# Optimization experiments

Hardware: AMD Instinct MI355X
Metric: run time of the kernel (lower is better)

Reference implementation:

```python
import jax, jax.numpy as jnp
import numpy as np

N, F, E, B, D = 100000, 256, 128, 10000, 32
GAMMA, ZETA = -0.1, 1.1  # hard-concrete stretch params of L0Dense


def setup_inputs() -> dict:
    key = jax.random.key(0)
    ks = jax.random.split(key, 12)
    return {
        "nodes": jax.random.randint(ks[0], (B,), 0, N),
        "neigh_idx": jax.random.randint(ks[1], (B, D), 0, N),
        "neigh_mask": jax.random.bernoulli(ks[2], 0.9, (B, D)),
        "feature": jax.random.normal(ks[3], (N, F), jnp.float32),
        "W": jax.random.normal(ks[4], (F, E), jnp.float32) * 0.05,
        "b": jnp.zeros((E,), jnp.float32),
        "qz_loga": jax.random.normal(ks[5], (F,), jnp.float32),
        "att1_w": jax.random.normal(ks[6], (2 * E, E), jnp.float32) * 0.05,
        "att1_b": jnp.zeros((E,), jnp.float32),
        "att2_w": jax.random.normal(ks[7], (E, E), jnp.float32) * 0.05,
        "att2_b": jnp.zeros((E,), jnp.float32),
        "att3_w": jax.random.normal(ks[8], (E, 1), jnp.float32) * 0.05,
        "att3_b": jnp.zeros((1,), jnp.float32),
    }


def reference(nodes, neigh_idx, neigh_mask, feature, W, b, qz_loga,
              att1_w, att1_b, att2_w, att2_b, att3_w, att3_b):
    # L0Dense, deterministic (eval) hard-concrete gate on input dims
    z = jnp.clip(jax.nn.sigmoid(qz_loga) * (ZETA - GAMMA) + GAMMA, 0.0, 1.0)
    We = W * z[:, None]                                  # [F, E]

    node_feat = feature[nodes] @ We + b                   # [B, E]
    neigh_feat = feature[neigh_idx] @ We + b              # [B, D, E]

    # GraphRec-style attention MLP over (neighbor, center) pairs
    h = jnp.concatenate(
        [neigh_feat, jnp.broadcast_to(node_feat[:, None, :], neigh_feat.shape)],
        axis=-1)                                          # [B, D, 2E]
    h = jax.nn.relu(h @ att1_w + att1_b)
    h = jax.nn.relu(h @ att2_w + att2_b)
    scores = (h @ att3_w + att3_b)[..., 0]                # [B, D]
    scores = jnp.where(neigh_mask, scores, -1e30)
    att = jax.nn.softmax(scores, axis=-1)                 # [B, D]

    agg = jnp.einsum('bd,bde->be', att, neigh_feat)       # weighted sum
    has_neigh = neigh_mask.any(axis=-1, keepdims=True)
    return jnp.where(has_neigh, agg, node_feat)           # n==0 fallback
```

## Files before the change

kernel.cpp:

```cpp
#include <hip/hip_runtime.h>
#include <hip/hip_bf16.h>
#include <math.h>

#define NN 100000
#define FF 256
#define EE 128
#define BB_ 10000
#define DD 32

typedef __attribute__((ext_vector_type(8))) short short8;
typedef __attribute__((ext_vector_type(4))) float f32x4;

__device__ __forceinline__ short f2bf(float f) {
  __hip_bfloat16 h = __float2bfloat16(f);
  union { __hip_bfloat16 h; short s; } u; u.h = h;
  return u.s;
}
__device__ __forceinline__ float bf2f(short s) {
  union { unsigned u; float f; } v;
  v.u = ((unsigned)(unsigned short)s) << 16;
  return v.f;
}

__global__ __launch_bounds__(256) void k_prep(
    const float* __restrict__ W, const float* __restrict__ qz,
    const float* __restrict__ a1w, const float* __restrict__ a2w,
    short* __restrict__ WeT, short* __restrict__ a1wTn,
    short* __restrict__ a1wTc, short* __restrict__ w2T) {
  int i = blockIdx.x * 256 + threadIdx.x;
  if (i < 32768) {
    int e = i >> 8, f = i & 255;
    float g = qz[f];
    float s = 1.0f / (1.0f + expf(-g));
    float z = fminf(fmaxf(s * 1.2f - 0.1f, 0.0f), 1.0f);
    WeT[e * 256 + f] = f2bf(W[f * 128 + e] * z);
  } else if (i < 49152) {
    int t = i - 32768; int n = t >> 7, k = t & 127;
    a1wTn[n * 128 + k] = f2bf(a1w[k * 128 + n]);
  } else if (i < 65536) {
    int t = i - 49152; int n = t >> 7, k = t & 127;
    a1wTc[n * 128 + k] = f2bf(a1w[(128 + k) * 128 + n]);
  } else if (i < 81920) {
    int t = i - 65536; int n = t >> 7, k = t & 127;
    w2T[n * 128 + k] = f2bf(a2w[k * 128 + n]);
  }
}

template <int K, bool AF32, bool OUTBF16>
__global__ __launch_bounds__(256) void k_mm(
    const void* __restrict__ Ap, const short* __restrict__ BT,
    const float* __restrict__ bias, const int* __restrict__ idx,
    void* __restrict__ Cp, int M) {
  __shared__ short As[128 * 64];
  __shared__ short Bs[128 * 64];
  const int tid = threadIdx.x;
  const int mb = blockIdx.x * 128;
  const int wave = tid >> 6, lane = tid & 63;
  const int wr = wave >> 1, wc = wave & 1;
  const int l15 = lane & 15, lg = lane >> 4;

  size_t abase[4];
#pragma unroll
  for (int s = 0; s < 4; ++s) {
    int row = (tid + s * 256) >> 3;
    int grow = mb + row;
    int gr = 0;
    if (grow < M) gr = idx ? idx[grow] : grow;
    abase[s] = (size_t)gr * K;
  }

  f32x4 acc[4][4];
#pragma unroll
  for (int i = 0; i < 4; ++i)
#pragma unroll
    for (int j = 0; j < 4; ++j) acc[i][j] = (f32x4){0.f, 0.f, 0.f, 0.f};

  for (int k0 = 0; k0 < K; k0 += 64) {
#pragma unroll
    for (int s = 0; s < 4; ++s) {
      int q = tid + s * 256;
      int row = q >> 3, c = q & 7;
      short8 av;
      if (AF32) {
        const float* ap = (const float*)Ap + abase[s] + k0 + c * 8;
        float4 f0 = *(const float4*)ap;
        float4 f1 = *(const float4*)(ap + 4);
        av[0] = f2bf(f0.x); av[1] = f2bf(f0.y);
        av[2] = f2bf(f0.z); av[3] = f2bf(f0.w);
        av[4] = f2bf(f1.x); av[5] = f2bf(f1.y);
        av[6] = f2bf(f1.z); av[7] = f2bf(f1.w);
      } else {
        av = *(const short8*)((const short*)Ap + abase[s] + k0 + c * 8);
      }
      *(short8*)(As + row * 64 + 8 * (c ^ (row & 7))) = av;
      short8 bv = *(const short8*)(BT + (size_t)row * K + k0 + c * 8);
      *(short8*)(Bs + row * 64 + 8 * (c ^ (row & 7))) = bv;
    }
    __syncthreads();
#pragma unroll
    for (int ks = 0; ks < 2; ++ks) {
      int c = ks * 4 + lg;
      short8 af[4], bfv[4];
#pragma unroll
      for (int i = 0; i < 4; ++i) {
        int r = wr * 64 + i * 16 + l15;
        af[i] = *(short8*)(As + r * 64 + 8 * (c ^ (r & 7)));
        int n = wc * 64 + i * 16 + l15;
        bfv[i] = *(short8*)(Bs + n * 64 + 8 * (c ^ (n & 7)));
      }
#pragma unroll
      for (int i = 0; i < 4; ++i)
#pragma unroll
        for (int j = 0; j < 4; ++j)
          acc[i][j] = __builtin_amdgcn_mfma_f32_16x16x32_bf16(
              af[i], bfv[j], acc[i][j], 0, 0, 0);
    }
    __syncthreads();
  }

  float bv4[4];
#pragma unroll
  for (int j = 0; j < 4; ++j) {
    int col = wc * 64 + j * 16 + l15;
    bv4[j] = bias ? bias[col] : 0.f;
  }
#pragma unroll
  for (int i = 0; i < 4; ++i) {
#pragma unroll
    for (int r = 0; r < 4; ++r) {
      int row = mb + wr * 64 + i * 16 + lg * 4 + r;
      if (row < M) {
#pragma unroll
        for (int j = 0; j < 4; ++j) {
          int col = wc * 64 + j * 16 + l15;
          float v = acc[i][j][r] + bv4[j];
          if (OUTBF16)
            ((short*)Cp)[(size_t)row * EE + col] = f2bf(v);
          else
            ((float*)Cp)[(size_t)row * EE + col] = v;
        }
      }
    }
  }
}

__global__ __launch_bounds__(256) void k_attn3(
    const short* __restrict__ X, const short* __restrict__ Y,
    const float* __restrict__ P, const int* __restrict__ nodes,
    const int* __restrict__ nidx, const int* __restrict__ nmask,
    const short* __restrict__ w2T, const float* __restrict__ b2,
    const float* __restrict__ w3, const float* __restrict__ b3,
    float* __restrict__ out) {
  __shared__ int ni_s[4][32];
  __shared__ float sc_s[4][32];
  __shared__ float att_s[4][32];
  const int tid = threadIdx.x;
  const int wave = tid >> 6, lane = tid & 63;
  const int b = blockIdx.x * 4 + wave;
  const int l15 = lane & 15, lg = lane >> 4;

  if (lane < 32) ni_s[wave][lane] = nidx[b * DD + lane];

  const int nid0 = ni_s[wave][l15];
  const int nid1 = ni_s[wave][16 + l15];
  const short* yr0 = Y + (size_t)nid0 * EE;
  const short* yr1 = Y + (size_t)nid1 * EE;
  const float* pr = P + (size_t)b * EE;

  f32x4 acc[2][8];
#pragma unroll
  for (int i = 0; i < 2; ++i)
#pragma unroll
    for (int j = 0; j < 8; ++j) acc[i][j] = (f32x4){0.f, 0.f, 0.f, 0.f};

#pragma unroll
  for (int ks = 0; ks < 4; ++ks) {
    const int k0 = ks * 32 + lg * 8;
    short8 y0 = *(const short8*)(yr0 + k0);
    short8 y1 = *(const short8*)(yr1 + k0);
    float4 pa = *(const float4*)(pr + k0);
    float4 pb = *(const float4*)(pr + k0 + 4);
    float pf[8] = {pa.x, pa.y, pa.z, pa.w, pb.x, pb.y, pb.z, pb.w};
    short8 a0, a1;
#pragma unroll
    for (int e = 0; e < 8; ++e) {
      a0[e] = f2bf(fmaxf(bf2f(y0[e]) + pf[e], 0.f));
      a1[e] = f2bf(fmaxf(bf2f(y1[e]) + pf[e], 0.f));
    }
    short8 bfv[8];
#pragma unroll
    for (int j = 0; j < 8; ++j)
      bfv[j] = *(const short8*)(w2T + (size_t)(j * 16 + l15) * EE + k0);
    __builtin_amdgcn_s_setprio(1);
#pragma unroll
    for (int j = 0; j < 8; ++j) {
      acc[0][j] = __builtin_amdgcn_mfma_f32_16x16x32_bf16(a0, bfv[j],
                                                          acc[0][j], 0, 0, 0);
      acc[1][j] = __builtin_amdgcn_mfma_f32_16x16x32_bf16(a1, bfv[j],
                                                          acc[1][j], 0, 0, 0);
    }
    __builtin_amdgcn_s_setprio(0);
  }

  float b2v[8], w3v[8];
#pragma unroll
  for (int j = 0; j < 8; ++j) {
    int col = j * 16 + l15;
    b2v[j] = b2[col];
    w3v[j] = w3[col];
  }
  float part[2][4];
#pragma unroll
  for (int i = 0; i < 2; ++i)
#pragma unroll
    for (int r = 0; r < 4; ++r) {
      float s = 0.f;
#pragma unroll
      for (int j = 0; j < 8; ++j)
        s += fmaxf(acc[i][j][r] + b2v[j], 0.f) * w3v[j];
      part[i][r] = s;
    }
#pragma unroll
  for (int off = 1; off <= 8; off <<= 1) {
#pragma unroll
    for (int i = 0; i < 2; ++i)
#pragma unroll
      for (int r = 0; r < 4; ++r) part[i][r] += __shfl_xor(part[i][r], off);
  }
  if (l15 == 0) {
#pragma unroll
    for (int i = 0; i < 2; ++i)
#pragma unroll
      for (int r = 0; r < 4; ++r)
        sc_s[wave][i * 16 + lg * 4 + r] = part[i][r];
  }

  const int row = lane & 31;
  const int m = nmask[(size_t)b * DD + row];
  float s = sc_s[wave][row] + b3[0];
  if (!m) s = -1e30f;
  float mx = s;
#pragma unroll
  for (int off = 1; off <= 16; off <<= 1) mx = fmaxf(mx, __shfl_xor(mx, off));
  float e = expf(s - mx);
  float sum = e;
#pragma unroll
  for (int off = 1; off <= 16; off <<= 1) sum += __shfl_xor(sum, off);
  if (lane < 32) att_s[wave][row] = e / sum;
  const bool has = (__ballot(m != 0) != 0ull);

  float a0 = 0.f, a1 = 0.f;
  if (has) {
#pragma unroll 4
    for (int d = 0; d < 32; ++d) {
      float a = att_s[wave][d];
      const short* xr = X + (size_t)ni_s[wave][d] * EE;
      unsigned xv = *(const unsigned*)(xr + 2 * lane);
      a0 += a * bf2f((short)(xv & 0xffffu));
      a1 += a * bf2f((short)(xv >> 16));
    }
  } else {
    const short* xr = X + (size_t)nodes[b] * EE;
    unsigned xv = *(const unsigned*)(xr + 2 * lane);
    a0 = bf2f((short)(xv & 0xffffu));
    a1 = bf2f((short)(xv >> 16));
  }
  *(float2*)(out + (size_t)b * EE + 2 * lane) = make_float2(a0, a1);
}

extern "C" void kernel_launch(void* const* d_in, const int* in_sizes, int n_in,
                              void* d_out, int out_size, void* d_ws,
                              size_t ws_size, hipStream_t stream) {
  const int* nodes = (const int*)d_in[0];
  const int* nidx = (const int*)d_in[1];
  const int* nmask = (const int*)d_in[2];
  const float* feature = (const float*)d_in[3];
  const float* W = (const float*)d_in[4];
  const float* bb = (const float*)d_in[5];
  const float* qz = (const float*)d_in[6];
  const float* a1w = (const float*)d_in[7];
  const float* a1b = (const float*)d_in[8];
  const float* a2w = (const float*)d_in[9];
  const float* a2b = (const float*)d_in[10];
  const float* a3w = (const float*)d_in[11];
  const float* a3b = (const float*)d_in[12];
  float* out = (float*)d_out;

  char* ws = (char*)d_ws;
  short* WeT   = (short*)(ws);
  short* a1wTn = (short*)(ws + 65536);
  short* a1wTc = (short*)(ws + 98304);
  short* w2T   = (short*)(ws + 131072);
  short* Xb    = (short*)(ws + 163840);
  short* Yb    = (short*)(ws + 163840 + 25600000);
  float* Pv    = (float*)(ws + 163840 + 51200000);

  k_prep<<<320, 256, 0, stream>>>(W, qz, a1w, a2w, WeT, a1wTn, a1wTc, w2T);
  k_mm<256, true, true><<<(NN + 127) / 128, 256, 0, stream>>>(
      feature, WeT, bb, nullptr, Xb, NN);
  k_mm<128, false, true><<<(NN + 127) / 128, 256, 0, stream>>>(
      Xb, a1wTn, a1b, nullptr, Yb, NN);
  k_mm<128, false, false><<<(BB_ + 127) / 128, 256, 0, stream>>>(
      Xb, a1wTc, nullptr, nodes, Pv, BB_);
  k_attn3<<<BB_ / 4, 256, 0, stream>>>(Xb, Yb, Pv, nodes, nidx, nmask, w2T,
                                       a2b, a3w, a3b, out);
}
```

Baseline: 130.4 us.

## Fold attention layer-1 neighbor weights into feature GEMM via composed weights

Precomputes a composed weight matrix (We @ att1_w neighbor half) and its bias so one GEMM over the fp32 feature table produces both X and Y in an interleaved 256-wide bf16 buffer. This drops the separate X→Y GEMM pass, which re-read and re-wrote the full N×128 table. The attention kernel now also preloads all 32 neighbor X rows into registers up front to overlap gathers with the MFMA work. In exchange, Y is computed from fp32 features instead of bf16-rounded X, which changes rounding slightly, and the larger register footprint may lower occupancy.

New measurement: 137.2 us. 1.05x slower.

```diff
diff --git a/kernel.cpp b/kernel.cpp
--- a/kernel.cpp
+++ b/kernel.cpp
@@ -25,28 +25,48 @@
 __global__ __launch_bounds__(256) void k_prep(
     const float* __restrict__ W, const float* __restrict__ qz,
     const float* __restrict__ a1w, const float* __restrict__ a2w,
-    short* __restrict__ WeT, short* __restrict__ a1wTn,
-    short* __restrict__ a1wTc, short* __restrict__ w2T) {
+    const float* __restrict__ bb,
+    float* __restrict__ Wef32, short* __restrict__ BT2,
+    short* __restrict__ a1wTc, short* __restrict__ w2T,
+    float* __restrict__ bias2) {
   int i = blockIdx.x * 256 + threadIdx.x;
   if (i < 32768) {
-    int e = i >> 8, f = i & 255;
+    int f = i >> 7, e = i & 127;
     float g = qz[f];
     float s = 1.0f / (1.0f + expf(-g));
     float z = fminf(fmaxf(s * 1.2f - 0.1f, 0.0f), 1.0f);
-    WeT[e * 256 + f] = f2bf(W[f * 128 + e] * z);
+    float v = W[f * 128 + e] * z;
+    Wef32[f * 128 + e] = v;
+    BT2[e * 256 + f] = f2bf(v);
   } else if (i < 49152) {
     int t = i - 32768; int n = t >> 7, k = t & 127;
-    a1wTn[n * 128 + k] = f2bf(a1w[k * 128 + n]);
+    a1wTc[n * 128 + k] = f2bf(a1w[(128 + k) * 128 + n]);
   } else if (i < 65536) {
     int t = i - 49152; int n = t >> 7, k = t & 127;
-    a1wTc[n * 128 + k] = f2bf(a1w[(128 + k) * 128 + n]);
-  } else if (i < 81920) {
-    int t = i - 65536; int n = t >> 7, k = t & 127;
     w2T[n * 128 + k] = f2bf(a2w[k * 128 + n]);
-  }
-}
-
-template <int K, bool AF32, bool OUTBF16>
+  } else if (i < 65664) {
+    bias2[i - 65536] = bb[i - 65536];
+  }
+}
+
+__global__ __launch_bounds__(256) void k_compose(
+    const float* __restrict__ Wef32, const float* __restrict__ a1w,
+    const float* __restrict__ a1b, const float* __restrict__ bb,
+    short* __restrict__ BT2, float* __restrict__ bias2) {
+  const int n = blockIdx.x;
+  const int f = threadIdx.x;
+  float s = 0.f;
+  for (int e = 0; e < 128; ++e)
+    s = fmaf(a1w[e * 128 + n], Wef32[f * 128 + e], s);
+  BT2[(size_t)(128 + n) * 256 + f] = f2bf(s);
+  if (f == 0) {
+    float by = a1b[n];
+    for (int e = 0; e < 128; ++e) by = fmaf(bb[e], a1w[e * 128 + n], by);
+    bias2[128 + n] = by;
+  }
+}
+
+template <int K, int LDA, int LDC, bool AF32, bool OUTBF16>
 __global__ __launch_bounds__(256) void k_mm(
     const void* __restrict__ Ap, const short* __restrict__ BT,
     const float* __restrict__ bias, const int* __restrict__ idx,
@@ -55,6 +75,7 @@
   __shared__ short Bs[128 * 64];
   const int tid = threadIdx.x;
   const int mb = blockIdx.x * 128;
+  const int col0 = blockIdx.y * 128;
   const int wave = tid >> 6, lane = tid & 63;
   const int wr = wave >> 1, wc = wave & 1;
   const int l15 = lane & 15, lg = lane >> 4;
@@ -66,7 +87,7 @@
     int grow = mb + row;
     int gr = 0;
     if (grow < M) gr = idx ? idx[grow] : grow;
-    abase[s] = (size_t)gr * K;
+    abase[s] = (size_t)gr * LDA;
   }
 
   f32x4 acc[4][4];
@@ -93,7 +114,7 @@
         av = *(const short8*)((const short*)Ap + abase[s] + k0 + c * 8);
       }
       *(short8*)(As + row * 64 + 8 * (c ^ (row & 7))) = av;
-      short8 bv = *(const short8*)(BT + (size_t)row * K + k0 + c * 8);
+      short8 bv = *(const short8*)(BT + (size_t)(col0 + row) * K + k0 + c * 8);
       *(short8*)(Bs + row * 64 + 8 * (c ^ (row & 7))) = bv;
     }
     __syncthreads();
@@ -122,7 +143,7 @@
 #pragma unroll
   for (int j = 0; j < 4; ++j) {
     int col = wc * 64 + j * 16 + l15;
-    bv4[j] = bias ? bias[col] : 0.f;
+    bv4[j] = bias ? bias[col0 + col] : 0.f;
   }
 #pragma unroll
   for (int i = 0; i < 4; ++i) {
@@ -135,22 +156,21 @@
           int col = wc * 64 + j * 16 + l15;
           float v = acc[i][j][r] + bv4[j];
           if (OUTBF16)
-            ((short*)Cp)[(size_t)row * EE + col] = f2bf(v);
+            ((short*)Cp)[(size_t)row * LDC + col0 + col] = f2bf(v);
           else
-            ((float*)Cp)[(size_t)row * EE + col] = v;
+            ((float*)Cp)[(size_t)row * LDC + col0 + col] = v;
         }
       }
     }
   }
 }
 
-__global__ __launch_bounds__(256) void k_attn3(
-    const short* __restrict__ X, const short* __restrict__ Y,
-    const float* __restrict__ P, const int* __restrict__ nodes,
-    const int* __restrict__ nidx, const int* __restrict__ nmask,
-    const short* __restrict__ w2T, const float* __restrict__ b2,
-    const float* __restrict__ w3, const float* __restrict__ b3,
-    float* __restrict__ out) {
+__global__ __launch_bounds__(256) void k_attn4(
+    const short* __restrict__ XY, const float* __restrict__ P,
+    const int* __restrict__ nodes, const int* __restrict__ nidx,
+    const int* __restrict__ nmask, const short* __restrict__ w2T,
+    const float* __restrict__ b2, const float* __restrict__ w3,
+    const float* __restrict__ b3, float* __restrict__ out) {
   __shared__ int ni_s[4][32];
   __shared__ float sc_s[4][32];
   __shared__ float att_s[4][32];
@@ -161,31 +181,42 @@
 
   if (lane < 32) ni_s[wave][lane] = nidx[b * DD + lane];
 
+  const int m = nmask[(size_t)b * DD + (lane & 31)];
   const int nid0 = ni_s[wave][l15];
   const int nid1 = ni_s[wave][16 + l15];
-  const short* yr0 = Y + (size_t)nid0 * EE;
-  const short* yr1 = Y + (size_t)nid1 * EE;
-  const float* pr = P + (size_t)b * EE;
-
-  f32x4 acc[2][8];
-#pragma unroll
-  for (int i = 0; i < 2; ++i)
-#pragma unroll
-    for (int j = 0; j < 8; ++j) acc[i][j] = (f32x4){0.f, 0.f, 0.f, 0.f};
-
+  const short* yr0 = XY + (size_t)nid0 * 256 + 128;
+  const short* yr1 = XY + (size_t)nid1 * 256 + 128;
+  short8 y0v[4], y1v[4];
 #pragma unroll
   for (int ks = 0; ks < 4; ++ks) {
     const int k0 = ks * 32 + lg * 8;
-    short8 y0 = *(const short8*)(yr0 + k0);
-    short8 y1 = *(const short8*)(yr1 + k0);
+    y0v[ks] = *(const short8*)(yr0 + k0);
+    y1v[ks] = *(const short8*)(yr1 + k0);
+  }
+  unsigned xv[32];
+#pragma unroll
+  for (int d = 0; d < 32; ++d)
+    xv[d] = *(const unsigned*)(XY + (size_t)ni_s[wave][d] * 256 + 2 * lane);
+
+  const float* pr = P + (size_t)b * EE;
+
+  f32x4 acc[2][8];
+#pragma unroll
+  for (int i = 0; i < 2; ++i)
+#pragma unroll
+    for (int j = 0; j < 8; ++j) acc[i][j] = (f32x4){0.f, 0.f, 0.f, 0.f};
+
+#pragma unroll
+  for (int ks = 0; ks < 4; ++ks) {
+    const int k0 = ks * 32 + lg * 8;
     float4 pa = *(const float4*)(pr + k0);
     float4 pb = *(const float4*)(pr + k0 + 4);
     float pf[8] = {pa.x, pa.y, pa.z, pa.w, pb.x, pb.y, pb.z, pb.w};
     short8 a0, a1;
 #pragma unroll
     for (int e = 0; e < 8; ++e) {
-      a0[e] = f2bf(fmaxf(bf2f(y0[e]) + pf[e], 0.f));
-      a1[e] = f2bf(fmaxf(bf2f(y1[e]) + pf[e], 0.f));
+      a0[e] = f2bf(fmaxf(bf2f(y0v[ks][e]) + pf[e], 0.f));
+      a1[e] = f2bf(fmaxf(bf2f(y1v[ks][e]) + pf[e], 0.f));
     }
     short8 bfv[8];
 #pragma unroll
@@ -236,7 +267,6 @@
   }
 
   const int row = lane & 31;
-  const int m = nmask[(size_t)b * DD + row];
   float s = sc_s[wave][row] + b3[0];
   if (!m) s = -1e30f;
   float mx = s;
@@ -251,19 +281,17 @@
 
   float a0 = 0.f, a1 = 0.f;
   if (has) {
-#pragma unroll 4
+#pragma unroll
     for (int d = 0; d < 32; ++d) {
       float a = att_s[wave][d];
-      const short* xr = X + (size_t)ni_s[wave][d] * EE;
-      unsigned xv = *(const unsigned*)(xr + 2 * lane);
-      a0 += a * bf2f((short)(xv & 0xffffu));
-      a1 += a * bf2f((short)(xv >> 16));
+      a0 += a * bf2f((short)(xv[d] & 0xffffu));
+      a1 += a * bf2f((short)(xv[d] >> 16));
     }
   } else {
-    const short* xr = X + (size_t)nodes[b] * EE;
-    unsigned xv = *(const unsigned*)(xr + 2 * lane);
-    a0 = bf2f((short)(xv & 0xffffu));
-    a1 = bf2f((short)(xv >> 16));
+    const short* xr = XY + (size_t)nodes[b] * 256;
+    unsigned x2 = *(const unsigned*)(xr + 2 * lane);
+    a0 = bf2f((short)(x2 & 0xffffu));
+    a1 = bf2f((short)(x2 >> 16));
   }
   *(float2*)(out + (size_t)b * EE + 2 * lane) = make_float2(a0, a1);
 }
@@ -287,21 +315,23 @@
   float* out = (float*)d_out;
 
   char* ws = (char*)d_ws;
-  short* WeT   = (short*)(ws);
-  short* a1wTn = (short*)(ws + 65536);
-  short* a1wTc = (short*)(ws + 98304);
-  short* w2T   = (short*)(ws + 131072);
-  short* Xb    = (short*)(ws + 163840);
-  short* Yb    = (short*)(ws + 163840 + 25600000);
-  float* Pv    = (float*)(ws + 163840 + 51200000);
-
-  k_prep<<<320, 256, 0, stream>>>(W, qz, a1w, a2w, WeT, a1wTn, a1wTc, w2T);
-  k_mm<256, true, true><<<(NN + 127) / 128, 256, 0, stream>>>(
-      feature, WeT, bb, nullptr, Xb, NN);
-  k_mm<128, false, true><<<(NN + 127) / 128, 256, 0, stream>>>(
-      Xb, a1wTn, a1b, nullptr, Yb, NN);
-  k_mm<128, false, false><<<(BB_ + 127) / 128, 256, 0, stream>>>(
-      Xb, a1wTc, nullptr, nodes, Pv, BB_);
-  k_attn3<<<BB_ / 4, 256, 0, stream>>>(Xb, Yb, Pv, nodes, nidx, nmask, w2T,
-                                       a2b, a3w, a3b, out);
-}
+  short* BT2   = (short*)(ws);
+  float* Wef32 = (float*)(ws + 131072);
+  short* a1wTc = (short*)(ws + 262144);
+  short* w2T   = (short*)(ws + 294912);
+  float* bias2 = (float*)(ws + 327680);
+  short* XYb   = (short*)(ws + 524288);
+  float* Pv    = (float*)(ws + 524288 + 51200000);
+
+  k_prep<<<257, 256, 0, stream>>>(W, qz, a1w, a2w, bb, Wef32, BT2, a1wTc, w2T,
+                                  bias2);
+  k_compose<<<128, 256, 0, stream>>>(Wef32, a1w, a1b, bb, BT2, bias2);
+  k_mm<256, 256, 256, true, true><<<dim3((NN + 127) / 128, 2), 256, 0,
+                                    stream>>>(feature, BT2, bias2, nullptr,
+                                              XYb, NN);
+  k_mm<128, 256, 128, false, false><<<dim3((BB_ + 127) / 128, 1), 256, 0,
+                                      stream>>>(XYb, a1wTc, nullptr, nodes, Pv,
+                                                BB_);
+  k_attn4<<<BB_ / 4, 256, 0, stream>>>(XYb, Pv, nodes, nidx, nmask, w2T, a2b,
+                                       a3w, a3b, out);
+}
```
